# Kernel tuning notes

Hardware: AMD Instinct MI355X
Metric: run time of the kernel (lower is better)

Reference implementation:

```python
import jax, jax.numpy as jnp
import numpy as np

B, C, H, W = 2048, 4, 64, 64
K = 3  # shift / patch kernel size


def _l2_normalize(x, axis=-1, eps=1e-12):
    n = jnp.linalg.norm(x, axis=axis, keepdims=True)
    return x / jnp.maximum(n, eps)


def _circular_convolution(weights, kernel):
    # weights: [B,H,W], kernel: [B,3,3] (softmax-normalized shift kernel)
    res = jnp.zeros_like(weights)
    c = K // 2
    for dh in range(K):
        for dw in range(K):
            coeff = kernel[:, dh, dw][:, None, None]
            res = res + coeff * jnp.roll(weights, shift=(dh - c, dw - c), axis=(1, 2))
    return res


def _apply_patch(weights, patch):
    # weights: [B,H,W], patch: [B,C,3,3] -> [B,C,H,W]; zero-padded (non-circular) shifts
    c = K // 2
    wp = jnp.pad(weights, ((0, 0), (c, c), (c, c)))  # [B,H+2,W+2]
    res = jnp.zeros((weights.shape[0], patch.shape[1], H, W), dtype=weights.dtype)
    for dh in range(K):
        for dw in range(K):
            coeff = patch[:, :, dh, dw][:, :, None, None]  # [B,C,1,1]
            # result[y,x] += patch[dh,dw] * weights[y-(dh-c), x-(dw-c)] within bounds
            win = wp[:, 2 * c - dh:2 * c - dh + H, 2 * c - dw:2 * c - dw + W]  # [B,H,W]
            res = res + coeff * win[:, None, :, :]
    return res


def setup_inputs() -> dict:
    key = jax.random.key(0)
    ks = jax.random.split(key, 12)
    return {
        "map_state": jax.random.uniform(ks[0], (B, C, H, W), dtype=jnp.float32),
        "weight_state": jnp.ones((B, H, W), dtype=jnp.float32) / float(H * W),
        "key": jax.random.normal(ks[1], (B, C), dtype=jnp.float32),
        "beta": jax.random.normal(ks[2], (B, 1), dtype=jnp.float32),
        "gate": jax.random.normal(ks[3], (B, 1), dtype=jnp.float32),
        "shift": jax.random.normal(ks[4], (B, K * K), dtype=jnp.float32),
        "sharpen": jax.random.normal(ks[5], (B, 1), dtype=jnp.float32),
        "erase": jax.random.normal(ks[6], (B, C), dtype=jnp.float32),
        "add": jax.random.normal(ks[7], (B, C), dtype=jnp.float32),
        "add_patch_logits": jax.random.normal(ks[8], (B, C, K, K), dtype=jnp.float32),
        "erase_patch_logits": jax.random.normal(ks[9], (B, C, K, K), dtype=jnp.float32),
    }


def reference(map_state, weight_state, key, beta, gate, shift, sharpen, erase, add,
              add_patch_logits, erase_patch_logits):
    b = map_state.shape[0]
    # content addressing: cosine similarity against flattened memory
    flat_mem = map_state.reshape(b, C, H * W).transpose(0, 2, 1)  # [B,HW,C]
    key_norm = _l2_normalize(key)                                  # [B,C]
    mem_norm = _l2_normalize(flat_mem)                             # [B,HW,C]
    similarity = jnp.einsum('bnc,bc->bn', mem_norm, key_norm)      # [B,HW]
    beta_pos = jax.nn.softplus(beta) + 1e-6                        # [B,1]
    content_w = jax.nn.softmax(beta_pos * similarity, axis=-1)
    # interpolation gate with previous weights
    gate_sigma = jax.nn.sigmoid(gate)                              # [B,1]
    prev_w = weight_state.reshape(b, -1)
    gated = gate_sigma * content_w + (1.0 - gate_sigma) * prev_w
    # differentiable circular shift
    shift_kernel = jax.nn.softmax(shift, axis=-1).reshape(b, K, K)
    shifted = _circular_convolution(gated.reshape(b, H, W), shift_kernel)
    # sharpening
    sharpen_pos = 1.0 + jax.nn.softplus(sharpen)                   # [B,1]
    sharpened = jnp.clip(shifted, 1e-6, None).reshape(b, -1) ** sharpen_pos
    weights = sharpened / (jnp.sum(sharpened, axis=-1, keepdims=True) + 1e-6)
    weights = weights / (jnp.sum(weights, axis=-1, keepdims=True) + 1e-6)
    weights_2d = weights.reshape(b, H, W)
    # patch-based write (add + erase)
    add_patch = jax.nn.sigmoid(add_patch_logits)
    erase_patch = jax.nn.sigmoid(erase_patch_logits)
    add_map = _apply_patch(weights_2d, add_patch)
    erase_map = jnp.clip(_apply_patch(weights_2d, erase_patch), 0.0, 1.0)
    map_updated = map_state * (1.0 - erase_map) + add_map
    read_vector = jnp.sum(map_updated * weights_2d[:, None, :, :], axis=(2, 3))  # [B,C]
    return map_updated, weights_2d, read_vector
```

## Files before the change

kernel.cpp:

```cpp
#include <hip/hip_runtime.h>
#include <math.h>

#define CC 4
#define HH 64
#define WW 64
#define NN (HH*WW)
#define NTH 256
#define GRP 4
#define LDW 65

#if __has_builtin(__builtin_amdgcn_exp2f)
#define FEXP2(x) __builtin_amdgcn_exp2f(x)
#else
#define FEXP2(x) exp2f(x)
#endif
#if __has_builtin(__builtin_amdgcn_logf)
#define FLOG2(x) __builtin_amdgcn_logf(x)
#else
#define FLOG2(x) log2f(x)
#endif
#define LOG2E 1.4426950408889634f

__device__ __forceinline__ float softplusf(float x) {
    return (x > 20.f) ? x : log1pf(expf(x));
}
__device__ __forceinline__ float sigmoidf(float x) {
    return 1.f / (1.f + expf(-x));
}

__device__ __forceinline__ float bred(float v, float* sc, bool do_max) {
#pragma unroll
    for (int o = 32; o > 0; o >>= 1) {
        float other = __shfl_down(v, o, 64);
        v = do_max ? fmaxf(v, other) : (v + other);
    }
    if ((threadIdx.x & 63) == 0) sc[threadIdx.x >> 6] = v;
    __syncthreads();
    return do_max ? fmaxf(fmaxf(sc[0], sc[1]), fmaxf(sc[2], sc[3]))
                  : ((sc[0] + sc[1]) + (sc[2] + sc[3]));
}

__global__ __launch_bounds__(NTH)
void slam_kernel(const float* __restrict__ map_state,
                 const float* __restrict__ weight_state,
                 const float* __restrict__ key,
                 const float* __restrict__ beta,
                 const float* __restrict__ gate,
                 const float* __restrict__ shift,
                 const float* __restrict__ sharpen,
                 const float* __restrict__ add_patch_logits,
                 const float* __restrict__ erase_patch_logits,
                 float* __restrict__ out_map,
                 float* __restrict__ out_w,
                 float* __restrict__ out_rv)
{
    __shared__ float sw[HH * LDW];
    __shared__ float spatch[2 * CC * 9];
    __shared__ float sks[9];
    __shared__ float sred[8][4];

    const int b = blockIdx.x;
    const int tid = threadIdx.x;

    const float* keyb = key + b * CC;
    float k0 = keyb[0], k1 = keyb[1], k2 = keyb[2], k3 = keyb[3];
    {
        float inv = rsqrtf(fmaxf(k0*k0 + k1*k1 + k2*k2 + k3*k3, 1e-24f));
        k0 *= inv; k1 *= inv; k2 *= inv; k3 *= inv;
    }
    const float beta_pos  = softplusf(beta[b]) + 1e-6f;
    const float g         = sigmoidf(gate[b]);
    const float sharp_pos = 1.f + softplusf(sharpen[b]);

    if (tid == 0) {
        const float* sh = shift + b * 9;
        float m = sh[0];
#pragma unroll
        for (int i = 1; i < 9; ++i) m = fmaxf(m, sh[i]);
        float s = 0.f;
        float e[9];
#pragma unroll
        for (int i = 0; i < 9; ++i) { e[i] = FEXP2((sh[i] - m) * LOG2E); s += e[i]; }
        float inv = 1.f / s;
#pragma unroll
        for (int i = 0; i < 9; ++i) sks[i] = e[i] * inv;
    }

    if (tid < 2 * CC * 9) {
        float v = (tid < CC * 9) ? add_patch_logits[b * CC * 9 + tid]
                                 : erase_patch_logits[b * CC * 9 + (tid - CC * 9)];
        spatch[tid] = sigmoidf(v);
    }

    const float4* mp4 = (const float4*)(map_state    + (size_t)b * CC * NN);
    const float4* pw4 = (const float4*)(weight_state + (size_t)b * NN);
    float4*       om4 = (float4*)(out_map + (size_t)b * CC * NN);
    float4*       ow4 = (float4*)(out_w   + (size_t)b * NN);

    float lmax = -INFINITY;
#pragma unroll 1
    for (int gix = 0; gix < GRP; ++gix) {
        const int base = tid + gix * NTH;
        const int P = 4 * base, h = P >> 6, w0 = P & 63;
        float4 mv0 = mp4[base];
        float4 mv1 = mp4[(NN/4) + base];
        float4 mv2 = mp4[2*(NN/4) + base];
        float4 mv3 = mp4[3*(NN/4) + base];
        float* row = sw + h * LDW + w0;
#pragma unroll
        for (int j = 0; j < 4; ++j) {
            float a0 = ((const float*)&mv0)[j];
            float a1 = ((const float*)&mv1)[j];
            float a2 = ((const float*)&mv2)[j];
            float a3 = ((const float*)&mv3)[j];
            float inv = rsqrtf(fmaxf(a0*a0 + a1*a1 + a2*a2 + a3*a3, 1e-24f));
            float zz = beta_pos * (a0*k0 + a1*k1 + a2*k2 + a3*k3) * inv;
            row[j] = zz;
            lmax = fmaxf(lmax, zz);
        }
    }
    const float zmax = bred(lmax, sred[0], true);

    float lsum = 0.f;
#pragma unroll 1
    for (int gix = 0; gix < GRP; ++gix) {
        const int base = tid + gix * NTH;
        const int P = 4 * base, h = P >> 6, w0 = P & 63;
        const float* row = sw + h * LDW + w0;
#pragma unroll
        for (int j = 0; j < 4; ++j)
            lsum += FEXP2((row[j] - zmax) * LOG2E);
    }
    const float Z = bred(lsum, sred[1], false);
    const float gZinv = g / Z;
    const float g1 = 1.f - g;

#pragma unroll 1
    for (int gix = 0; gix < GRP; ++gix) {
        const int base = tid + gix * NTH;
        const int P = 4 * base, h = P >> 6, w0 = P & 63;
        float4 pw = pw4[base];
        float* row = sw + h * LDW + w0;
#pragma unroll
        for (int j = 0; j < 4; ++j) {
            float e = FEXP2((row[j] - zmax) * LOG2E);
            row[j] = gZinv * e + g1 * ((const float*)&pw)[j];
        }
    }
    __syncthreads();

    float z[16];
    float lsum1 = 0.f;
#pragma unroll
    for (int gix = 0; gix < GRP; ++gix) {
        const int P = 4 * (tid + gix * NTH), h = P >> 6, w0 = P & 63;
        const int rr[3] = { (h + 1) & 63, h, (h + 63) & 63 };
        const int cm = (w0 + 63) & 63, cp = (w0 + 4) & 63;
        float acc0 = 0.f, acc1 = 0.f, acc2 = 0.f, acc3 = 0.f;
#pragma unroll
        for (int dh = 0; dh < 3; ++dh) {
            const float* rp = sw + rr[dh] * LDW;
            float b0 = rp[cm];
            float b1 = rp[w0];
            float b2 = rp[w0 + 1];
            float b3 = rp[w0 + 2];
            float b4 = rp[w0 + 3];
            float b5 = rp[cp];
            float s0 = sks[dh*3+0], s1 = sks[dh*3+1], s2 = sks[dh*3+2];
            acc0 += s0*b2 + s1*b1 + s2*b0;
            acc1 += s0*b3 + s1*b2 + s2*b1;
            acc2 += s0*b4 + s1*b3 + s2*b2;
            acc3 += s0*b5 + s1*b4 + s2*b3;
        }
        float p0 = FEXP2(sharp_pos * FLOG2(fmaxf(acc0, 1e-6f)));
        float p1 = FEXP2(sharp_pos * FLOG2(fmaxf(acc1, 1e-6f)));
        float p2 = FEXP2(sharp_pos * FLOG2(fmaxf(acc2, 1e-6f)));
        float p3 = FEXP2(sharp_pos * FLOG2(fmaxf(acc3, 1e-6f)));
        z[gix*4+0] = p0; z[gix*4+1] = p1; z[gix*4+2] = p2; z[gix*4+3] = p3;
        lsum1 += (p0 + p1) + (p2 + p3);
    }
    const float S1 = bred(lsum1, sred[2], false);
    const float inv1 = 1.f / (S1 + 1e-6f);
    const float S2 = S1 * inv1;
    const float scale = inv1 / (S2 + 1e-6f);

#pragma unroll
    for (int gix = 0; gix < GRP; ++gix) {
        const int base = tid + gix * NTH;
        const int P = 4 * base, h = P >> 6, w0 = P & 63;
        float* row = sw + h * LDW + w0;
        float4 o;
#pragma unroll
        for (int j = 0; j < 4; ++j) {
            float wv = z[gix*4 + j] * scale;
            row[j] = wv;
            ((float*)&o)[j] = wv;
        }
        ow4[base] = o;
    }
    __syncthreads();

    float rv[CC] = {0.f, 0.f, 0.f, 0.f};
#pragma unroll 1
    for (int gix = 0; gix < GRP; ++gix) {
        const int base = tid + gix * NTH;
        const int P = 4 * base, h = P >> 6, w0 = P & 63;
        float buf[3][6];
#pragma unroll
        for (int dh = 0; dh < 3; ++dh) {
            const int r = h + 1 - dh;
            if ((unsigned)r < (unsigned)HH) {
                const float* rp = sw + r * LDW;
                buf[dh][0] = (w0 > 0) ? rp[w0 - 1] : 0.f;
                buf[dh][1] = rp[w0];
                buf[dh][2] = rp[w0 + 1];
                buf[dh][3] = rp[w0 + 2];
                buf[dh][4] = rp[w0 + 3];
                buf[dh][5] = (w0 + 4 < WW) ? rp[w0 + 4] : 0.f;
            } else {
#pragma unroll
                for (int k = 0; k < 6; ++k) buf[dh][k] = 0.f;
            }
        }
        const float wn0 = buf[1][1], wn1 = buf[1][2], wn2 = buf[1][3], wn3 = buf[1][4];
#pragma unroll
        for (int ch = 0; ch < CC; ++ch) {
            float4 m4 = mp4[ch * (NN/4) + base];
            float a0 = 0.f, a1 = 0.f, a2 = 0.f, a3 = 0.f;
            float e0 = 0.f, e1 = 0.f, e2 = 0.f, e3 = 0.f;
#pragma unroll
            for (int dh = 0; dh < 3; ++dh) {
#pragma unroll
                for (int t = 0; t < 3; ++t) {
                    const float ca = spatch[ch * 9 + dh * 3 + t];
                    const float ce = spatch[CC * 9 + ch * 9 + dh * 3 + t];
                    a0 += ca * buf[dh][2 - t];  e0 += ce * buf[dh][2 - t];
                    a1 += ca * buf[dh][3 - t];  e1 += ce * buf[dh][3 - t];
                    a2 += ca * buf[dh][4 - t];  e2 += ce * buf[dh][4 - t];
                    a3 += ca * buf[dh][5 - t];  e3 += ce * buf[dh][5 - t];
                }
            }
            float4 o;
            float mu;
            mu = ((const float*)&m4)[0] * (1.f - fminf(fmaxf(e0, 0.f), 1.f)) + a0;
            ((float*)&o)[0] = mu; rv[ch] += mu * wn0;
            mu = ((const float*)&m4)[1] * (1.f - fminf(fmaxf(e1, 0.f), 1.f)) + a1;
            ((float*)&o)[1] = mu; rv[ch] += mu * wn1;
            mu = ((const float*)&m4)[2] * (1.f - fminf(fmaxf(e2, 0.f), 1.f)) + a2;
            ((float*)&o)[2] = mu; rv[ch] += mu * wn2;
            mu = ((const float*)&m4)[3] * (1.f - fminf(fmaxf(e3, 0.f), 1.f)) + a3;
            ((float*)&o)[3] = mu; rv[ch] += mu * wn3;
            om4[ch * (NN/4) + base] = o;
        }
    }

#pragma unroll
    for (int c = 0; c < CC; ++c) {
        float v = rv[c];
#pragma unroll
        for (int o = 32; o > 0; o >>= 1) v += __shfl_down(v, o, 64);
        if ((tid & 63) == 0) sred[4 + c][tid >> 6] = v;
    }
    __syncthreads();
    if (tid == 0) {
#pragma unroll
        for (int c = 0; c < CC; ++c)
            out_rv[(size_t)b * CC + c] =
                (sred[4+c][0] + sred[4+c][1]) + (sred[4+c][2] + sred[4+c][3]);
    }
}

extern "C" void kernel_launch(void* const* d_in, const int* in_sizes, int n_in,
                              void* d_out, int out_size, void* d_ws, size_t ws_size,
                              hipStream_t stream) {
    const float* map_state          = (const float*)d_in[0];
    const float* weight_state       = (const float*)d_in[1];
    const float* key                = (const float*)d_in[2];
    const float* beta               = (const float*)d_in[3];
    const float* gate               = (const float*)d_in[4];
    const float* shift              = (const float*)d_in[5];
    const float* sharpen            = (const float*)d_in[6];
    const float* add_patch_logits   = (const float*)d_in[9];
    const float* erase_patch_logits = (const float*)d_in[10];

    const int B = in_sizes[1] / NN;

    float* out_map = (float*)d_out;
    float* out_w   = out_map + (size_t)B * CC * NN;
    float* out_rv  = out_w   + (size_t)B * NN;

    slam_kernel<<<B, NTH, 0, stream>>>(map_state, weight_state, key, beta, gate,
                                       shift, sharpen, add_patch_logits,
                                       erase_patch_logits, out_map, out_w, out_rv);
}
```

Baseline: 96.25 us.

## Use 1024-thread blocks with one float4 group per thread, keeping values in registers

Result: slower. 103.2 us (+7.2%).

```diff
diff --git a/kernel.cpp b/kernel.cpp
--- a/kernel.cpp
+++ b/kernel.cpp
@@ -5,8 +5,8 @@
 #define HH 64
 #define WW 64
 #define NN (HH*WW)
-#define NTH 256
-#define GRP 4
+#define NTH 1024
+#define NW (NTH/64)
 #define LDW 65
 
 #if __has_builtin(__builtin_amdgcn_exp2f)
@@ -36,8 +36,15 @@
     }
     if ((threadIdx.x & 63) == 0) sc[threadIdx.x >> 6] = v;
     __syncthreads();
-    return do_max ? fmaxf(fmaxf(sc[0], sc[1]), fmaxf(sc[2], sc[3]))
-                  : ((sc[0] + sc[1]) + (sc[2] + sc[3]));
+    float r = sc[0];
+    if (do_max) {
+#pragma unroll
+        for (int i = 1; i < NW; ++i) r = fmaxf(r, sc[i]);
+    } else {
+#pragma unroll
+        for (int i = 1; i < NW; ++i) r += sc[i];
+    }
+    return r;
 }
 
 __global__ __launch_bounds__(NTH)
@@ -57,10 +64,14 @@
     __shared__ float sw[HH * LDW];
     __shared__ float spatch[2 * CC * 9];
     __shared__ float sks[9];
-    __shared__ float sred[8][4];
+    __shared__ float sred[8][NW];
 
     const int b = blockIdx.x;
     const int tid = threadIdx.x;
+
+    const int P  = 4 * tid;
+    const int h  = P >> 6;
+    const int w0 = P & 63;
 
     const float* keyb = key + b * CC;
     float k0 = keyb[0], k1 = keyb[1], k2 = keyb[2], k3 = keyb[3];
@@ -97,16 +108,14 @@
     float4*       om4 = (float4*)(out_map + (size_t)b * CC * NN);
     float4*       ow4 = (float4*)(out_w   + (size_t)b * NN);
 
+    float z[4];
+
     float lmax = -INFINITY;
-#pragma unroll 1
-    for (int gix = 0; gix < GRP; ++gix) {
-        const int base = tid + gix * NTH;
-        const int P = 4 * base, h = P >> 6, w0 = P & 63;
-        float4 mv0 = mp4[base];
-        float4 mv1 = mp4[(NN/4) + base];
-        float4 mv2 = mp4[2*(NN/4) + base];
-        float4 mv3 = mp4[3*(NN/4) + base];
-        float* row = sw + h * LDW + w0;
+    {
+        float4 mv0 = mp4[tid];
+        float4 mv1 = mp4[(NN/4) + tid];
+        float4 mv2 = mp4[2*(NN/4) + tid];
+        float4 mv3 = mp4[3*(NN/4) + tid];
 #pragma unroll
         for (int j = 0; j < 4; ++j) {
             float a0 = ((const float*)&mv0)[j];
@@ -115,45 +124,34 @@
             float a3 = ((const float*)&mv3)[j];
             float inv = rsqrtf(fmaxf(a0*a0 + a1*a1 + a2*a2 + a3*a3, 1e-24f));
             float zz = beta_pos * (a0*k0 + a1*k1 + a2*k2 + a3*k3) * inv;
-            row[j] = zz;
+            z[j] = zz;
             lmax = fmaxf(lmax, zz);
         }
     }
     const float zmax = bred(lmax, sred[0], true);
 
     float lsum = 0.f;
-#pragma unroll 1
-    for (int gix = 0; gix < GRP; ++gix) {
-        const int base = tid + gix * NTH;
-        const int P = 4 * base, h = P >> 6, w0 = P & 63;
-        const float* row = sw + h * LDW + w0;
-#pragma unroll
-        for (int j = 0; j < 4; ++j)
-            lsum += FEXP2((row[j] - zmax) * LOG2E);
+#pragma unroll
+    for (int j = 0; j < 4; ++j) {
+        float e = FEXP2((z[j] - zmax) * LOG2E);
+        z[j] = e;
+        lsum += e;
     }
     const float Z = bred(lsum, sred[1], false);
     const float gZinv = g / Z;
     const float g1 = 1.f - g;
 
-#pragma unroll 1
-    for (int gix = 0; gix < GRP; ++gix) {
-        const int base = tid + gix * NTH;
-        const int P = 4 * base, h = P >> 6, w0 = P & 63;
-        float4 pw = pw4[base];
+    {
+        float4 pw = pw4[tid];
         float* row = sw + h * LDW + w0;
 #pragma unroll
-        for (int j = 0; j < 4; ++j) {
-            float e = FEXP2((row[j] - zmax) * LOG2E);
-            row[j] = gZinv * e + g1 * ((const float*)&pw)[j];
-        }
-    }
-    __syncthreads();
-
-    float z[16];
+        for (int j = 0; j < 4; ++j)
+            row[j] = gZinv * z[j] + g1 * ((const float*)&pw)[j];
+    }
+    __syncthreads();
+
     float lsum1 = 0.f;
-#pragma unroll
-    for (int gix = 0; gix < GRP; ++gix) {
-        const int P = 4 * (tid + gix * NTH), h = P >> 6, w0 = P & 63;
+    {
         const int rr[3] = { (h + 1) & 63, h, (h + 63) & 63 };
         const int cm = (w0 + 63) & 63, cp = (w0 + 4) & 63;
         float acc0 = 0.f, acc1 = 0.f, acc2 = 0.f, acc3 = 0.f;
@@ -172,39 +170,32 @@
             acc2 += s0*b4 + s1*b3 + s2*b2;
             acc3 += s0*b5 + s1*b4 + s2*b3;
         }
-        float p0 = FEXP2(sharp_pos * FLOG2(fmaxf(acc0, 1e-6f)));
-        float p1 = FEXP2(sharp_pos * FLOG2(fmaxf(acc1, 1e-6f)));
-        float p2 = FEXP2(sharp_pos * FLOG2(fmaxf(acc2, 1e-6f)));
-        float p3 = FEXP2(sharp_pos * FLOG2(fmaxf(acc3, 1e-6f)));
-        z[gix*4+0] = p0; z[gix*4+1] = p1; z[gix*4+2] = p2; z[gix*4+3] = p3;
-        lsum1 += (p0 + p1) + (p2 + p3);
+        z[0] = FEXP2(sharp_pos * FLOG2(fmaxf(acc0, 1e-6f)));
+        z[1] = FEXP2(sharp_pos * FLOG2(fmaxf(acc1, 1e-6f)));
+        z[2] = FEXP2(sharp_pos * FLOG2(fmaxf(acc2, 1e-6f)));
+        z[3] = FEXP2(sharp_pos * FLOG2(fmaxf(acc3, 1e-6f)));
+        lsum1 = (z[0] + z[1]) + (z[2] + z[3]);
     }
     const float S1 = bred(lsum1, sred[2], false);
     const float inv1 = 1.f / (S1 + 1e-6f);
     const float S2 = S1 * inv1;
     const float scale = inv1 / (S2 + 1e-6f);
 
-#pragma unroll
-    for (int gix = 0; gix < GRP; ++gix) {
-        const int base = tid + gix * NTH;
-        const int P = 4 * base, h = P >> 6, w0 = P & 63;
+    {
         float* row = sw + h * LDW + w0;
         float4 o;
 #pragma unroll
         for (int j = 0; j < 4; ++j) {
-            float wv = z[gix*4 + j] * scale;
+            float wv = z[j] * scale;
             row[j] = wv;
             ((float*)&o)[j] = wv;
         }
-        ow4[base] = o;
-    }
-    __syncthreads();
-
-    float rv[CC] = {0.f, 0.f, 0.f, 0.f};
-#pragma unroll 1
-    for (int gix = 0; gix < GRP; ++gix) {
-        const int base = tid + gix * NTH;
-        const int P = 4 * base, h = P >> 6, w0 = P & 63;
+        ow4[tid] = o;
+    }
+    __syncthreads();
+
+    float rv0 = 0.f, rv1 = 0.f, rv2 = 0.f, rv3 = 0.f;
+    {
         float buf[3][6];
 #pragma unroll
         for (int dh = 0; dh < 3; ++dh) {
@@ -225,7 +216,7 @@
         const float wn0 = buf[1][1], wn1 = buf[1][2], wn2 = buf[1][3], wn3 = buf[1][4];
 #pragma unroll
         for (int ch = 0; ch < CC; ++ch) {
-            float4 m4 = mp4[ch * (NN/4) + base];
+            float4 m4 = mp4[ch * (NN/4) + tid];
             float a0 = 0.f, a1 = 0.f, a2 = 0.f, a3 = 0.f;
             float e0 = 0.f, e1 = 0.f, e2 = 0.f, e3 = 0.f;
 #pragma unroll
@@ -243,30 +234,41 @@
             float4 o;
             float mu;
             mu = ((const float*)&m4)[0] * (1.f - fminf(fmaxf(e0, 0.f), 1.f)) + a0;
-            ((float*)&o)[0] = mu; rv[ch] += mu * wn0;
+            ((float*)&o)[0] = mu;
+            float acc = mu * wn0;
             mu = ((const float*)&m4)[1] * (1.f - fminf(fmaxf(e1, 0.f), 1.f)) + a1;
-            ((float*)&o)[1] = mu; rv[ch] += mu * wn1;
+            ((float*)&o)[1] = mu;
+            acc += mu * wn1;
             mu = ((const float*)&m4)[2] * (1.f - fminf(fmaxf(e2, 0.f), 1.f)) + a2;
-            ((float*)&o)[2] = mu; rv[ch] += mu * wn2;
+            ((float*)&o)[2] = mu;
+            acc += mu * wn2;
             mu = ((const float*)&m4)[3] * (1.f - fminf(fmaxf(e3, 0.f), 1.f)) + a3;
-            ((float*)&o)[3] = mu; rv[ch] += mu * wn3;
-            om4[ch * (NN/4) + base] = o;
-        }
-    }
-
-#pragma unroll
-    for (int c = 0; c < CC; ++c) {
-        float v = rv[c];
-#pragma unroll
-        for (int o = 32; o > 0; o >>= 1) v += __shfl_down(v, o, 64);
-        if ((tid & 63) == 0) sred[4 + c][tid >> 6] = v;
-    }
-    __syncthreads();
-    if (tid == 0) {
-#pragma unroll
-        for (int c = 0; c < CC; ++c)
-            out_rv[(size_t)b * CC + c] =
-                (sred[4+c][0] + sred[4+c][1]) + (sred[4+c][2] + sred[4+c][3]);
+            ((float*)&o)[3] = mu;
+            acc += mu * wn3;
+            om4[ch * (NN/4) + tid] = o;
+            if      (ch == 0) rv0 = acc;
+            else if (ch == 1) rv1 = acc;
+            else if (ch == 2) rv2 = acc;
+            else              rv3 = acc;
+        }
+    }
+
+    {
+        float v[4] = { rv0, rv1, rv2, rv3 };
+#pragma unroll
+        for (int c = 0; c < CC; ++c) {
+            float x = v[c];
+#pragma unroll
+            for (int o = 32; o > 0; o >>= 1) x += __shfl_down(x, o, 64);
+            if ((tid & 63) == 0) sred[4 + c][tid >> 6] = x;
+        }
+    }
+    __syncthreads();
+    if (tid < CC) {
+        float s = 0.f;
+#pragma unroll
+        for (int i = 0; i < NW; ++i) s += sred[4 + tid][i];
+        out_rv[(size_t)b * CC + tid] = s;
     }
 }
 
```

## Drop softmax max pass, stage sharpened weights in LDS, fold normalization into patch pass

Applied to the files above, without the earlier changes.

After: 87.88 us. -8.7%, faster.

```diff
diff --git a/kernel.cpp b/kernel.cpp
--- a/kernel.cpp
+++ b/kernel.cpp
@@ -7,6 +7,7 @@
 #define NN (HH*WW)
 #define NTH 256
 #define GRP 4
+#define NW (NTH/64)
 #define LDW 65
 
 #if __has_builtin(__builtin_amdgcn_exp2f)
@@ -19,25 +20,22 @@
 #else
 #define FLOG2(x) log2f(x)
 #endif
-#define LOG2E 1.4426950408889634f
-
-__device__ __forceinline__ float softplusf(float x) {
-    return (x > 20.f) ? x : log1pf(expf(x));
-}
-__device__ __forceinline__ float sigmoidf(float x) {
-    return 1.f / (1.f + expf(-x));
-}
-
-__device__ __forceinline__ float bred(float v, float* sc, bool do_max) {
-#pragma unroll
-    for (int o = 32; o > 0; o >>= 1) {
-        float other = __shfl_down(v, o, 64);
-        v = do_max ? fmaxf(v, other) : (v + other);
-    }
+#define LOG2E  1.4426950408889634f
+#define RLOG2E 0.6931471805599453f
+
+__device__ __forceinline__ float fast_softplus(float x) {
+    return (x > 20.f) ? x : FLOG2(1.f + FEXP2(x * LOG2E)) * RLOG2E;
+}
+__device__ __forceinline__ float fast_sigmoid(float x) {
+    return 1.f / (1.f + FEXP2(-x * LOG2E));
+}
+
+__device__ __forceinline__ float bred_sum(float v, float* sc) {
+#pragma unroll
+    for (int o = 32; o > 0; o >>= 1) v += __shfl_down(v, o, 64);
     if ((threadIdx.x & 63) == 0) sc[threadIdx.x >> 6] = v;
     __syncthreads();
-    return do_max ? fmaxf(fmaxf(sc[0], sc[1]), fmaxf(sc[2], sc[3]))
-                  : ((sc[0] + sc[1]) + (sc[2] + sc[3]));
+    return (sc[0] + sc[1]) + (sc[2] + sc[3]);
 }
 
 __global__ __launch_bounds__(NTH)
@@ -55,50 +53,64 @@
                  float* __restrict__ out_rv)
 {
     __shared__ float sw[HH * LDW];
+    __shared__ float sp[HH * LDW];
     __shared__ float spatch[2 * CC * 9];
     __shared__ float sks[9];
-    __shared__ float sred[8][4];
+    __shared__ float sscal[8];
+    __shared__ float sred[6][NW];
 
     const int b = blockIdx.x;
     const int tid = threadIdx.x;
-
-    const float* keyb = key + b * CC;
-    float k0 = keyb[0], k1 = keyb[1], k2 = keyb[2], k3 = keyb[3];
-    {
-        float inv = rsqrtf(fmaxf(k0*k0 + k1*k1 + k2*k2 + k3*k3, 1e-24f));
-        k0 *= inv; k1 *= inv; k2 *= inv; k3 *= inv;
-    }
-    const float beta_pos  = softplusf(beta[b]) + 1e-6f;
-    const float g         = sigmoidf(gate[b]);
-    const float sharp_pos = 1.f + softplusf(sharpen[b]);
-
-    if (tid == 0) {
-        const float* sh = shift + b * 9;
-        float m = sh[0];
-#pragma unroll
-        for (int i = 1; i < 9; ++i) m = fmaxf(m, sh[i]);
-        float s = 0.f;
-        float e[9];
-#pragma unroll
-        for (int i = 0; i < 9; ++i) { e[i] = FEXP2((sh[i] - m) * LOG2E); s += e[i]; }
-        float inv = 1.f / s;
-#pragma unroll
-        for (int i = 0; i < 9; ++i) sks[i] = e[i] * inv;
-    }
-
-    if (tid < 2 * CC * 9) {
-        float v = (tid < CC * 9) ? add_patch_logits[b * CC * 9 + tid]
-                                 : erase_patch_logits[b * CC * 9 + (tid - CC * 9)];
-        spatch[tid] = sigmoidf(v);
-    }
 
     const float4* mp4 = (const float4*)(map_state    + (size_t)b * CC * NN);
     const float4* pw4 = (const float4*)(weight_state + (size_t)b * NN);
     float4*       om4 = (float4*)(out_map + (size_t)b * CC * NN);
     float4*       ow4 = (float4*)(out_w   + (size_t)b * NN);
-
-    float lmax = -INFINITY;
-#pragma unroll 1
+    float4*       sp4 = (float4*)sp;
+
+    float4 pwst[GRP];
+#pragma unroll
+    for (int gix = 0; gix < GRP; ++gix) pwst[gix] = pw4[tid + gix * NTH];
+
+    if (tid == 0) {
+        const float* sh = shift + b * 9;
+        float m = sh[0];
+#pragma unroll
+        for (int i = 1; i < 9; ++i) m = fmaxf(m, sh[i]);
+        float e[9]; float s = 0.f;
+#pragma unroll
+        for (int i = 0; i < 9; ++i) { e[i] = FEXP2((sh[i] - m) * LOG2E); s += e[i]; }
+        float inv = 1.f / s;
+#pragma unroll
+        for (int i = 0; i < 9; ++i) sks[i] = e[i] * inv;
+    } else if (tid == 64) {
+        const float* kb = key + b * CC;
+        float a = kb[0], c = kb[1], d = kb[2], f = kb[3];
+        float inv = rsqrtf(fmaxf(a*a + c*c + d*d + f*f, 1e-24f));
+        sscal[0] = a*inv; sscal[1] = c*inv; sscal[2] = d*inv; sscal[3] = f*inv;
+    } else if (tid == 128) {
+        sscal[4] = fast_softplus(beta[b]) + 1e-6f;
+    } else if (tid == 129) {
+        sscal[5] = fast_sigmoid(gate[b]);
+    } else if (tid == 130) {
+        sscal[6] = 1.f + fast_softplus(sharpen[b]);
+    }
+    if (tid >= 184) {
+        const int i = tid - 184;
+        float v = (i < CC * 9) ? add_patch_logits[b * CC * 9 + i]
+                               : erase_patch_logits[b * CC * 9 + (i - CC * 9)];
+        spatch[i] = fast_sigmoid(v);
+    }
+#pragma unroll
+    for (int gix = 0; gix < GRP; ++gix) sp4[tid + gix * NTH] = pwst[gix];
+    __syncthreads();
+
+    const float k0 = sscal[0], k1 = sscal[1], k2 = sscal[2], k3 = sscal[3];
+    const float beta_pos = sscal[4], g = sscal[5], sharp_pos = sscal[6];
+    const float bL = beta_pos * LOG2E;
+
+    float lsum = 0.f;
+#pragma unroll 2
     for (int gix = 0; gix < GRP; ++gix) {
         const int base = tid + gix * NTH;
         const int P = 4 * base, h = P >> 6, w0 = P & 63;
@@ -114,46 +126,32 @@
             float a2 = ((const float*)&mv2)[j];
             float a3 = ((const float*)&mv3)[j];
             float inv = rsqrtf(fmaxf(a0*a0 + a1*a1 + a2*a2 + a3*a3, 1e-24f));
-            float zz = beta_pos * (a0*k0 + a1*k1 + a2*k2 + a3*k3) * inv;
-            row[j] = zz;
-            lmax = fmaxf(lmax, zz);
-        }
-    }
-    const float zmax = bred(lmax, sred[0], true);
-
-    float lsum = 0.f;
-#pragma unroll 1
-    for (int gix = 0; gix < GRP; ++gix) {
-        const int base = tid + gix * NTH;
-        const int P = 4 * base, h = P >> 6, w0 = P & 63;
-        const float* row = sw + h * LDW + w0;
-#pragma unroll
-        for (int j = 0; j < 4; ++j)
-            lsum += FEXP2((row[j] - zmax) * LOG2E);
-    }
-    const float Z = bred(lsum, sred[1], false);
+            float e = FEXP2(bL * (a0*k0 + a1*k1 + a2*k2 + a3*k3) * inv);
+            row[j] = e;
+            lsum += e;
+        }
+    }
+    const float Z = bred_sum(lsum, sred[0]);
     const float gZinv = g / Z;
     const float g1 = 1.f - g;
 
-#pragma unroll 1
-    for (int gix = 0; gix < GRP; ++gix) {
-        const int base = tid + gix * NTH;
-        const int P = 4 * base, h = P >> 6, w0 = P & 63;
-        float4 pw = pw4[base];
+#pragma unroll
+    for (int gix = 0; gix < GRP; ++gix) {
+        const int base = tid + gix * NTH;
+        const int P = 4 * base, h = P >> 6, w0 = P & 63;
+        float4 pw = sp4[base];
         float* row = sw + h * LDW + w0;
 #pragma unroll
-        for (int j = 0; j < 4; ++j) {
-            float e = FEXP2((row[j] - zmax) * LOG2E);
-            row[j] = gZinv * e + g1 * ((const float*)&pw)[j];
-        }
-    }
-    __syncthreads();
-
-    float z[16];
+        for (int j = 0; j < 4; ++j)
+            row[j] = gZinv * row[j] + g1 * ((const float*)&pw)[j];
+    }
+    __syncthreads();
+
     float lsum1 = 0.f;
 #pragma unroll
     for (int gix = 0; gix < GRP; ++gix) {
-        const int P = 4 * (tid + gix * NTH), h = P >> 6, w0 = P & 63;
+        const int base = tid + gix * NTH;
+        const int P = 4 * base, h = P >> 6, w0 = P & 63;
         const int rr[3] = { (h + 1) & 63, h, (h + 63) & 63 };
         const int cm = (w0 + 63) & 63, cp = (w0 + 4) & 63;
         float acc0 = 0.f, acc1 = 0.f, acc2 = 0.f, acc3 = 0.f;
@@ -172,35 +170,20 @@
             acc2 += s0*b4 + s1*b3 + s2*b2;
             acc3 += s0*b5 + s1*b4 + s2*b3;
         }
+        float* prow = sp + h * LDW + w0;
         float p0 = FEXP2(sharp_pos * FLOG2(fmaxf(acc0, 1e-6f)));
         float p1 = FEXP2(sharp_pos * FLOG2(fmaxf(acc1, 1e-6f)));
         float p2 = FEXP2(sharp_pos * FLOG2(fmaxf(acc2, 1e-6f)));
         float p3 = FEXP2(sharp_pos * FLOG2(fmaxf(acc3, 1e-6f)));
-        z[gix*4+0] = p0; z[gix*4+1] = p1; z[gix*4+2] = p2; z[gix*4+3] = p3;
+        prow[0] = p0; prow[1] = p1; prow[2] = p2; prow[3] = p3;
         lsum1 += (p0 + p1) + (p2 + p3);
     }
-    const float S1 = bred(lsum1, sred[2], false);
-    const float inv1 = 1.f / (S1 + 1e-6f);
-    const float S2 = S1 * inv1;
+    const float S1 = bred_sum(lsum1, sred[1]);
+    const float inv1  = 1.f / (S1 + 1e-6f);
+    const float S2    = S1 * inv1;
     const float scale = inv1 / (S2 + 1e-6f);
 
-#pragma unroll
-    for (int gix = 0; gix < GRP; ++gix) {
-        const int base = tid + gix * NTH;
-        const int P = 4 * base, h = P >> 6, w0 = P & 63;
-        float* row = sw + h * LDW + w0;
-        float4 o;
-#pragma unroll
-        for (int j = 0; j < 4; ++j) {
-            float wv = z[gix*4 + j] * scale;
-            row[j] = wv;
-            ((float*)&o)[j] = wv;
-        }
-        ow4[base] = o;
-    }
-    __syncthreads();
-
-    float rv[CC] = {0.f, 0.f, 0.f, 0.f};
+    float rv0 = 0.f, rv1 = 0.f, rv2 = 0.f, rv3 = 0.f;
 #pragma unroll 1
     for (int gix = 0; gix < GRP; ++gix) {
         const int base = tid + gix * NTH;
@@ -210,19 +193,25 @@
         for (int dh = 0; dh < 3; ++dh) {
             const int r = h + 1 - dh;
             if ((unsigned)r < (unsigned)HH) {
-                const float* rp = sw + r * LDW;
-                buf[dh][0] = (w0 > 0) ? rp[w0 - 1] : 0.f;
-                buf[dh][1] = rp[w0];
-                buf[dh][2] = rp[w0 + 1];
-                buf[dh][3] = rp[w0 + 2];
-                buf[dh][4] = rp[w0 + 3];
-                buf[dh][5] = (w0 + 4 < WW) ? rp[w0 + 4] : 0.f;
+                const float* rp = sp + r * LDW;
+                buf[dh][0] = (w0 > 0) ? rp[w0 - 1] * scale : 0.f;
+                buf[dh][1] = rp[w0]     * scale;
+                buf[dh][2] = rp[w0 + 1] * scale;
+                buf[dh][3] = rp[w0 + 2] * scale;
+                buf[dh][4] = rp[w0 + 3] * scale;
+                buf[dh][5] = (w0 + 4 < WW) ? rp[w0 + 4] * scale : 0.f;
             } else {
 #pragma unroll
                 for (int k = 0; k < 6; ++k) buf[dh][k] = 0.f;
             }
         }
         const float wn0 = buf[1][1], wn1 = buf[1][2], wn2 = buf[1][3], wn3 = buf[1][4];
+        {
+            float4 o;
+            ((float*)&o)[0] = wn0; ((float*)&o)[1] = wn1;
+            ((float*)&o)[2] = wn2; ((float*)&o)[3] = wn3;
+            ow4[base] = o;
+        }
 #pragma unroll
         for (int ch = 0; ch < CC; ++ch) {
             float4 m4 = mp4[ch * (NN/4) + base];
@@ -241,32 +230,34 @@
                 }
             }
             float4 o;
-            float mu;
+            float mu, acc;
             mu = ((const float*)&m4)[0] * (1.f - fminf(fmaxf(e0, 0.f), 1.f)) + a0;
-            ((float*)&o)[0] = mu; rv[ch] += mu * wn0;
+            ((float*)&o)[0] = mu; acc  = mu * wn0;
             mu = ((const float*)&m4)[1] * (1.f - fminf(fmaxf(e1, 0.f), 1.f)) + a1;
-            ((float*)&o)[1] = mu; rv[ch] += mu * wn1;
+            ((float*)&o)[1] = mu; acc += mu * wn1;
             mu = ((const float*)&m4)[2] * (1.f - fminf(fmaxf(e2, 0.f), 1.f)) + a2;
-            ((float*)&o)[2] = mu; rv[ch] += mu * wn2;
+            ((float*)&o)[2] = mu; acc += mu * wn2;
             mu = ((const float*)&m4)[3] * (1.f - fminf(fmaxf(e3, 0.f), 1.f)) + a3;
-            ((float*)&o)[3] = mu; rv[ch] += mu * wn3;
+            ((float*)&o)[3] = mu; acc += mu * wn3;
             om4[ch * (NN/4) + base] = o;
+            if      (ch == 0) rv0 += acc;
+            else if (ch == 1) rv1 += acc;
+            else if (ch == 2) rv2 += acc;
+            else              rv3 += acc;
         }
     }
 
 #pragma unroll
     for (int c = 0; c < CC; ++c) {
-        float v = rv[c];
+        float v = (c == 0) ? rv0 : (c == 1) ? rv1 : (c == 2) ? rv2 : rv3;
 #pragma unroll
         for (int o = 32; o > 0; o >>= 1) v += __shfl_down(v, o, 64);
-        if ((tid & 63) == 0) sred[4 + c][tid >> 6] = v;
-    }
-    __syncthreads();
-    if (tid == 0) {
-#pragma unroll
-        for (int c = 0; c < CC; ++c)
-            out_rv[(size_t)b * CC + c] =
-                (sred[4+c][0] + sred[4+c][1]) + (sred[4+c][2] + sred[4+c][3]);
+        if ((tid & 63) == 0) sred[2 + c][tid >> 6] = v;
+    }
+    __syncthreads();
+    if (tid < CC) {
+        out_rv[(size_t)b * CC + tid] =
+            (sred[2 + tid][0] + sred[2 + tid][1]) + (sred[2 + tid][2] + sred[2 + tid][3]);
     }
 }
 
```
